# Optimization experiments

Measured on AMD Instinct MI355X. Metric: run time of the kernel, lower is better.

## Reference

```python
import jax, jax.numpy as jnp
import numpy as np

S, H, I, E, K = 16384, 1024, 512, 64, 2
CAP = 640  # capacity per expert: ceil(S*K/E * 1.25)


def setup_inputs() -> dict:
    key = jax.random.key(0)
    k0, k1, k2, k3, k4 = jax.random.split(key, 5)
    x = jax.random.normal(k0, (S, H), jnp.float32)
    w_gate = jax.random.normal(k1, (H, E), jnp.float32) * 0.02
    wg = jax.random.normal(k2, (E, H, I), jnp.float32) * 0.02
    wu = jax.random.normal(k3, (E, H, I), jnp.float32) * 0.02
    wd = jax.random.normal(k4, (E, I, H), jnp.float32) * 0.02
    return {"x": x, "w_gate": w_gate, "wg": wg, "wu": wu, "wd": wd}


def reference(x, w_gate, wg, wu, wd):
    # --- gate (fp32) + softmax ---
    logits = x.astype(jnp.float32) @ w_gate                      # [S,E]
    prob = jax.nn.softmax(logits, axis=-1)
    topk_p, topk_e = jax.lax.top_k(prob, K)                      # [S,K]

    # --- capacity-based dispatch (token-major, route-minor order, as in torch loop) ---
    flat_e = topk_e.reshape(-1)                                  # [S*K]
    onehot = jax.nn.one_hot(flat_e, E, dtype=jnp.int32)          # [S*K,E]
    pos = jnp.cumsum(onehot, axis=0)[jnp.arange(S * K), flat_e] - 1  # slot within expert
    valid = pos < CAP                                            # [S*K]

    combine_w = jnp.where(valid.reshape(S, K), topk_p, 0.0)      # dropped -> 0 weight
    slot_idx = jnp.where(valid, flat_e * CAP + pos, E * CAP)     # dummy row for drops
    x_rep = jnp.repeat(x, K, axis=0)                             # [S*K,H], row i = x[i//K]
    y = jnp.zeros((E * CAP + 1, H), x.dtype).at[slot_idx].set(x_rep)[: E * CAP]
    dispatched = y.reshape(E, CAP, H)

    # --- per-expert SwiGLU MLP (grouped GEMMs) ---
    g = jnp.einsum("ech,ehi->eci", dispatched, wg)
    u = jnp.einsum("ech,ehi->eci", dispatched, wu)
    expert_out = jnp.einsum("eci,eih->ech", jax.nn.silu(g) * u, wd)  # [E,CAP,H]

    # --- normalize weights and combine (gather + weighted sum) ---
    cw = combine_w / jnp.clip(combine_w.sum(-1, keepdims=True), 1e-12, None)
    scatter_index = jnp.where(valid, flat_e * CAP + pos, -1).reshape(S, K)
    gathered = expert_out.reshape(E * CAP, H)[scatter_index]     # [S,K,H]; -1 wraps, weight=0
    out = jnp.einsum("sk,skh->sh", cw, gathered)                 # [S,H]

    router_loss = jnp.zeros((1,), jnp.float32)
    return out, cw, router_loss, logits
```

## Files before the change

### kernel.cpp

```cpp
#include <hip/hip_runtime.h>
#include <hip/hip_bf16.h>

constexpr int S_TOK = 16384;
constexpr int HDIM  = 1024;
constexpr int IDIM  = 512;
constexpr int NEXP  = 64;
constexpr int CAPC  = 640;
constexpr int NCHUNK = 128;

typedef __attribute__((ext_vector_type(8))) short bf16x8;
typedef __attribute__((ext_vector_type(4))) short short4v;
typedef __attribute__((ext_vector_type(16))) float f32x16;

__device__ __forceinline__ float bf2f(unsigned short u){
  return __uint_as_float(((unsigned)u) << 16);
}
__device__ __forceinline__ unsigned short f2bf(float f){
  unsigned u = __float_as_uint(f);
  return (unsigned short)((u + 0x7fffu + ((u >> 16) & 1u)) >> 16);
}
__device__ __forceinline__ unsigned pk2cvt(float a, float b){
  unsigned r;
  asm volatile("v_cvt_pk_bf16_f32 %0, %1, %2" : "=v"(r) : "v"(a), "v"(b));
  return r;
}
__device__ __forceinline__ void gload_lds16(const void* g, void* l){
  __builtin_amdgcn_global_load_lds((const __attribute__((address_space(1))) unsigned*)g,
                                   (__attribute__((address_space(3))) unsigned*)l, 16, 0, 0);
}
__device__ __forceinline__ unsigned ldsoff(const void* p){ return (unsigned)(size_t)p; }
__device__ __forceinline__ void trread2(unsigned addr, short4v& lo, short4v& hi){
  asm volatile("ds_read_b64_tr_b16 %0, %2\n\t"
               "ds_read_b64_tr_b16 %1, %2 offset:128"
               : "=&v"(lo), "=&v"(hi) : "v"(addr));
}

__global__ __launch_bounds__(256) void gate_kernel(
    const float* __restrict__ x, const float* __restrict__ wgate,
    float* __restrict__ logits_out, float* __restrict__ topk_p,
    int* __restrict__ flat_e, float* __restrict__ rl_out)
{
  __shared__ float xs[4][HDIM];
  const int w = threadIdx.x >> 6, lane = threadIdx.x & 63;
  const int tok = blockIdx.x * 4 + w;
  const float4* xr = (const float4*)(x + (size_t)tok * HDIM);
  float4* xd = (float4*)(&xs[w][0]);
#pragma unroll
  for (int j = 0; j < 4; ++j) xd[j * 64 + lane] = xr[j * 64 + lane];
  __syncthreads();
  float acc = 0.f;
#pragma unroll 8
  for (int h = 0; h < HDIM; ++h)
    acc = fmaf(xs[w][h], wgate[h * NEXP + lane], acc);
  logits_out[(size_t)tok * NEXP + lane] = acc;
  float m = acc;
#pragma unroll
  for (int d = 1; d < 64; d <<= 1) m = fmaxf(m, __shfl_xor(m, d));
  float p = expf(acc - m);
  float sum = p;
#pragma unroll
  for (int d = 1; d < 64; d <<= 1) sum += __shfl_xor(sum, d);
  float prob = p / sum;
  float v = prob; int idx = lane;
#pragma unroll
  for (int d = 1; d < 64; d <<= 1){
    float ov = __shfl_xor(v, d); int oi = __shfl_xor(idx, d);
    if (ov > v || (ov == v && oi < idx)){ v = ov; idx = oi; }
  }
  const int e1 = idx; const float p1 = v;
  v = (lane == e1) ? -1.f : prob; idx = lane;
#pragma unroll
  for (int d = 1; d < 64; d <<= 1){
    float ov = __shfl_xor(v, d); int oi = __shfl_xor(idx, d);
    if (ov > v || (ov == v && oi < idx)){ v = ov; idx = oi; }
  }
  if (lane == 0){
    flat_e[tok * 2]     = e1;  flat_e[tok * 2 + 1] = idx;
    topk_p[tok * 2]     = p1;  topk_p[tok * 2 + 1] = v;
  }
  if (tok == 0 && lane == 0) rl_out[0] = 0.f;
}

__global__ __launch_bounds__(256) void hist_kernel(const int* __restrict__ flat_e,
                                                   int* __restrict__ counts)
{
  __shared__ int hh[NEXP];
  const int t = threadIdx.x;
  if (t < NEXP) hh[t] = 0;
  __syncthreads();
  const int e = flat_e[blockIdx.x * 256 + t];
  atomicAdd(&hh[e], 1);
  __syncthreads();
  if (t < NEXP) counts[blockIdx.x * NEXP + t] = hh[t];
}

__global__ __launch_bounds__(256) void offsets_kernel(const int* __restrict__ counts,
                                                      int* __restrict__ offs,
                                                      int* __restrict__ etot)
{
  const int w = threadIdx.x >> 6, lane = threadIdx.x & 63;
  const int e = blockIdx.x * 4 + w;
  int v0 = counts[lane * NEXP + e];
  int v1 = counts[(64 + lane) * NEXP + e];
  int s0 = v0, s1 = v1;
#pragma unroll
  for (int d = 1; d < 64; d <<= 1){
    int n0 = __shfl_up(s0, d); if (lane >= d) s0 += n0;
    int n1 = __shfl_up(s1, d); if (lane >= d) s1 += n1;
  }
  const int tot0 = __shfl(s0, 63);
  offs[lane * NEXP + e]        = s0 - v0;
  offs[(64 + lane) * NEXP + e] = tot0 + s1 - v1;
  if (lane == 63) etot[e] = tot0 + s1;
}

__global__ __launch_bounds__(256) void place_kernel(
    const int* __restrict__ flat_e, const float* __restrict__ topk_p,
    const int* __restrict__ offs, int* __restrict__ entry_slot,
    int* __restrict__ token_of_slot, float* __restrict__ cw_out)
{
  __shared__ int es[256];
  __shared__ float wsh[256];
  const int t = threadIdx.x;
  const int i = blockIdx.x * 256 + t;
  const int e = flat_e[i];
  es[t] = e;
  __syncthreads();
  int local = 0;
  for (int j = 0; j < t; ++j) local += (es[j] == e);
  const int pos = offs[blockIdx.x * NEXP + e] + local;
  const bool valid = pos < CAPC;
  const int slot = e * CAPC + pos;
  entry_slot[i] = valid ? slot : -1;
  if (valid) token_of_slot[slot] = i >> 1;
  const float p = topk_p[i];
  wsh[t] = valid ? p : 0.f;
  __syncthreads();
  const float wme = wsh[t], wo = wsh[t ^ 1];
  cw_out[i] = wme / fmaxf(wme + wo, 1e-12f);
}

__global__ __launch_bounds__(256) void adisp_kernel(
    const float* __restrict__ x, const int* __restrict__ token_of_slot,
    const int* __restrict__ etot, unsigned short* __restrict__ adisp)
{
  const int slot = blockIdx.x;
  const int e = slot / CAPC, c = slot - e * CAPC;
  int cnt = etot[e]; if (cnt > CAPC) cnt = CAPC;
  if (c >= cnt) return;
  const int tok = token_of_slot[slot];
  const int t = threadIdx.x;
  float4 v = ((const float4*)(x + (size_t)tok * HDIM))[t];
  ushort4 o; o.x = f2bf(v.x); o.y = f2bf(v.y); o.z = f2bf(v.z); o.w = f2bf(v.w);
  ((ushort4*)(adisp + (size_t)slot * HDIM))[t] = o;
}


__global__ __launch_bounds__(512, 2) void gemm1_kernel(
    const unsigned short* __restrict__ adisp,
    const float* __restrict__ wg, const float* __restrict__ wu,
    const int* __restrict__ etot,
    unsigned short* __restrict__ hbuf)
{
  constexpr int NK1 = HDIM / 32;
  __shared__ unsigned short As[3][128 * 32];
  __shared__ unsigned short Bs[3][2 * 128 * 32];
  const int bb = blockIdx.x;
  const int lb = (bb & 7) * 160 + (bb >> 3);
  const int e = lb / 20; const int r2 = lb - e * 20;
  const int nt = r2 / 5, mt = r2 - nt * 5;
  { int cnt = etot[e]; if (cnt > CAPC) cnt = CAPC;
    if (mt * 128 >= cnt) return; }
  const int t = threadIdx.x, w = t >> 6, lane = t & 63;
  const int wr = w >> 2, wc = w & 3;
  const size_t arow0 = (size_t)e * CAPC + (size_t)mt * 128;
  const unsigned short* abase = adisp + arow0 * HDIM;
  const float* gsrc = wg + (size_t)e * HDIM * IDIM + nt * 128;
  const float* usrc = wu + (size_t)e * HDIM * IDIM + nt * 128;

  int aoff; { int row = t >> 2, jsrc = (t & 3) ^ ((row >> 1) & 3);
              aoff = row * HDIM + jsrc * 8; }
  const int ks_ = w >> 2, khalf = (w >> 1) & 1, par = w & 1;
  const int dk = (lane >> 1) & 3, h8 = lane & 1;
  const int n16 = (lane >> 3) & 1, n32 = lane >> 4;
  const int bk = 16 * ks_ + 8 * khalf + 4 * par + dk;
  const int bn0 = n32 * 32 + n16 * 16 + h8 * 8;
  const int bgo = bk * IDIM + bn0;
  const unsigned bwo = (unsigned)(n32 * 1024 + ks_ * 512 + (khalf * 2 + n16) * 128
                                  + par * 64 + dk * 16 + h8 * 8);

  f32x16 ag[2], au[2];
#pragma unroll
  for (int i = 0; i < 2; ++i)
#pragma unroll
    for (int q = 0; q < 16; ++q){ ag[i][q] = 0.f; au[i][q] = 0.f; }

  float4 g0a, g0b, u0a, u0b, g1a, g1b, u1a, u1b;

#define G1_LOAD(KB, RA, RB, RC, RD) {                                          \
    const float* gp_ = gsrc + (size_t)(KB) * IDIM + bgo;                       \
    const float* up_ = usrc + (size_t)(KB) * IDIM + bgo;                       \
    RA = *(const float4*)gp_;       RB = *(const float4*)(gp_ + 4);            \
    RC = *(const float4*)up_;       RD = *(const float4*)(up_ + 4); }

#define G1_STORE(NB, WA, WB, WC, WD) {                                         \
    *(uint4*)&Bs[NB][bwo] = make_uint4(pk2cvt(WA.x,WA.y), pk2cvt(WA.z,WA.w),   \
                                       pk2cvt(WB.x,WB.y), pk2cvt(WB.z,WB.w));  \
    *(uint4*)&Bs[NB][4096 + bwo] = make_uint4(pk2cvt(WC.x,WC.y), pk2cvt(WC.z,WC.w), \
                                       pk2cvt(WD.x,WD.y), pk2cvt(WD.z,WD.w)); }

#define G1_STEP(TI, LA, LB, LC, LD, WA, WB, WC, WD) {                          \
    const int cur_ = (TI) % 3;                                                 \
    const bool pf_ = (TI) + 2 < NK1;                                           \
    if (pf_){                                                                  \
      const int kb2_ = ((TI) + 2) * 32;                                        \
      gload_lds16(abase + aoff + kb2_, &As[((TI) + 2) % 3][w * 64 * 8]);       \
      G1_LOAD(kb2_, LA, LB, LC, LD);                                           \
    }                                                                          \
    const unsigned b0_ = ldsoff(&Bs[cur_][0]) + (unsigned)wc * 2048            \
                         + (unsigned)(lane >> 4) * 256 + (unsigned)(lane & 15) * 8; \
    _Pragma("unroll")                                                          \
    for (int ksi = 0; ksi < 2; ++ksi){                                         \
      bf16x8 af0_, af1_, bg_, bu_;                                             \
      { int row0_ = wr * 64 + (lane & 31);                                     \
        int row1_ = row0_ + 32;                                                \
        int koct_ = ksi * 2 + (lane >> 5);                                     \
        af0_ = *(const bf16x8*)&As[cur_][row0_ * 32 + ((koct_ ^ ((row0_ >> 1) & 3)) * 8)]; \
        af1_ = *(const bf16x8*)&As[cur_][row1_ * 32 + ((koct_ ^ ((row1_ >> 1) & 3)) * 8)]; } \
      { short4v l0_, l1_, m0_, m1_;                                            \
        trread2(b0_ + (unsigned)ksi * 1024, l0_, l1_);                         \
        bg_ = __builtin_shufflevector(l0_, l1_, 0,1,2,3,4,5,6,7);              \
        trread2(b0_ + 8192 + (unsigned)ksi * 1024, m0_, m1_);                  \
        bu_ = __builtin_shufflevector(m0_, m1_, 0,1,2,3,4,5,6,7); }            \
      asm volatile("s_waitcnt lgkmcnt(0)" ::: "memory");                       \
      __builtin_amdgcn_sched_barrier(0);                                       \
      __builtin_amdgcn_s_setprio(1);                                           \
      ag[0] = __builtin_amdgcn_mfma_f32_32x32x16_bf16(af0_, bg_, ag[0], 0, 0, 0); \
      au[0] = __builtin_amdgcn_mfma_f32_32x32x16_bf16(af0_, bu_, au[0], 0, 0, 0); \
      ag[1] = __builtin_amdgcn_mfma_f32_32x32x16_bf16(af1_, bg_, ag[1], 0, 0, 0); \
      au[1] = __builtin_amdgcn_mfma_f32_32x32x16_bf16(af1_, bu_, au[1], 0, 0, 0); \
      __builtin_amdgcn_s_setprio(0);                                           \
    }                                                                          \
    if ((TI) + 1 < NK1){                                                       \
      if (pf_) asm volatile("s_waitcnt vmcnt(5)" ::: "memory");                \
      else     asm volatile("s_waitcnt vmcnt(0)" ::: "memory");                \
      G1_STORE(((TI) + 1) % 3, WA, WB, WC, WD);                                \
    }                                                                          \
    asm volatile("s_waitcnt lgkmcnt(0)" ::: "memory");                         \
    __builtin_amdgcn_s_barrier();                                              \
    __builtin_amdgcn_sched_barrier(0);                                         \
  }

  gload_lds16(abase + aoff + 0,  &As[0][w * 64 * 8]);
  G1_LOAD(0,  g0a, g0b, u0a, u0b);
  gload_lds16(abase + aoff + 32, &As[1][w * 64 * 8]);
  G1_LOAD(32, g1a, g1b, u1a, u1b);
  asm volatile("s_waitcnt vmcnt(5)" ::: "memory");
  G1_STORE(0, g0a, g0b, u0a, u0b);
  asm volatile("s_waitcnt lgkmcnt(0)" ::: "memory");
  __builtin_amdgcn_s_barrier();

  for (int tb = 0; tb < NK1; tb += 2){
    G1_STEP(tb,     g0a, g0b, u0a, u0b,  g1a, g1b, u1a, u1b);
    G1_STEP(tb + 1, g1a, g1b, u1a, u1b,  g0a, g0b, u0a, u0b);
  }
#undef G1_STEP
#undef G1_STORE
#undef G1_LOAD

#pragma unroll
  for (int mp = 0; mp < 2; ++mp)
#pragma unroll
    for (int r = 0; r < 16; ++r){
      int row = wr * 64 + mp * 32 + (r & 3) + 8 * (r >> 2) + 4 * (lane >> 5);
      int col = nt * 128 + wc * 32 + (lane & 31);
      float gv = ag[mp][r], uv = au[mp][r];
      float hv = gv / (1.f + expf(-gv)) * uv;
      hbuf[(arow0 + row) * IDIM + col] = f2bf(hv);
    }
}

__global__ __launch_bounds__(512, 2) void gemm2_kernel(
    const unsigned short* __restrict__ hbuf,
    const float* __restrict__ wd,
    const int* __restrict__ etot,
    unsigned short* __restrict__ eo)
{
  constexpr int NK2 = IDIM / 32;
  __shared__ unsigned short As[3][128 * 32];
  __shared__ unsigned short Bs[3][2 * 128 * 32];
  const int bb = blockIdx.x;
  const int lb = (bb & 7) * 160 + (bb >> 3);
  const int e = lb / 20; const int r2 = lb - e * 20;
  const int nt = r2 / 5, mt = r2 - nt * 5;
  { int cnt = etot[e]; if (cnt > CAPC) cnt = CAPC;
    if (mt * 128 >= cnt) return; }
  const int t = threadIdx.x, w = t >> 6, lane = t & 63;
  const int wr = w >> 2, wc = w & 3;
  const size_t arow0 = (size_t)e * CAPC + (size_t)mt * 128;
  const unsigned short* abase = hbuf + arow0 * IDIM;
  const float* dsrc = wd + (size_t)e * IDIM * HDIM + nt * 256;

  int aoff; { int row = t >> 2, jsrc = (t & 3) ^ ((row >> 1) & 3);
              aoff = row * IDIM + jsrc * 8; }
  const int ks_ = w >> 2, khalf = (w >> 1) & 1, par = w & 1;
  const int dk = (lane >> 1) & 3, h8 = lane & 1;
  const int n16 = (lane >> 3) & 1, n32 = lane >> 4;
  const int bk = 16 * ks_ + 8 * khalf + 4 * par + dk;
  const int bn0 = n32 * 32 + n16 * 16 + h8 * 8;
  const int bgo = bk * HDIM + bn0;
  const unsigned bwo = (unsigned)(n32 * 1024 + ks_ * 512 + (khalf * 2 + n16) * 128
                                  + par * 64 + dk * 16 + h8 * 8);

  f32x16 ac[2][2];
#pragma unroll
  for (int i = 0; i < 2; ++i)
#pragma unroll
    for (int j = 0; j < 2; ++j)
#pragma unroll
      for (int q = 0; q < 16; ++q) ac[i][j][q] = 0.f;

  float4 p0a, p0b, p1a, p1b, q0a, q0b, q1a, q1b;

#define G2_LOAD(KB, RA, RB, RC, RD) {                                          \
    const float* gp_ = dsrc + (size_t)(KB) * HDIM + bgo;                       \
    RA = *(const float4*)gp_;         RB = *(const float4*)(gp_ + 4);          \
    RC = *(const float4*)(gp_ + 128); RD = *(const float4*)(gp_ + 132); }

#define G2_STORE(NB, WA, WB, WC, WD) {                                         \
    *(uint4*)&Bs[NB][bwo] = make_uint4(pk2cvt(WA.x,WA.y), pk2cvt(WA.z,WA.w),   \
                                       pk2cvt(WB.x,WB.y), pk2cvt(WB.z,WB.w));  \
    *(uint4*)&Bs[NB][4096 + bwo] = make_uint4(pk2cvt(WC.x,WC.y), pk2cvt(WC.z,WC.w), \
                                       pk2cvt(WD.x,WD.y), pk2cvt(WD.z,WD.w)); }

#define G2_STEP(TI, LA, LB, LC, LD, WA, WB, WC, WD) {                          \
    const int cur_ = (TI) % 3;                                                 \
    const bool pf_ = (TI) + 2 < NK2;                                           \
    if (pf_){                                                                  \
      const int kb2_ = ((TI) + 2) * 32;                                        \
      gload_lds16(abase + aoff + kb2_, &As[((TI) + 2) % 3][w * 64 * 8]);       \
      G2_LOAD(kb2_, LA, LB, LC, LD);                                           \
    }                                                                          \
    const unsigned b0_ = ldsoff(&Bs[cur_][0]) + (unsigned)wc * 4096            \
                         + (unsigned)(lane >> 4) * 256 + (unsigned)(lane & 15) * 8; \
    _Pragma("unroll")                                                          \
    for (int ksi = 0; ksi < 2; ++ksi){                                         \
      bf16x8 af0_, af1_, b0f_, b1f_;                                           \
      { int row0_ = wr * 64 + (lane & 31);                                     \
        int row1_ = row0_ + 32;                                                \
        int koct_ = ksi * 2 + (lane >> 5);                                     \
        af0_ = *(const bf16x8*)&As[cur_][row0_ * 32 + ((koct_ ^ ((row0_ >> 1) & 3)) * 8)]; \
        af1_ = *(const bf16x8*)&As[cur_][row1_ * 32 + ((koct_ ^ ((row1_ >> 1) & 3)) * 8)]; } \
      { short4v l0_, l1_, m0_, m1_;                                            \
        trread2(b0_ + (unsigned)ksi * 1024, l0_, l1_);                         \
        b0f_ = __builtin_shufflevector(l0_, l1_, 0,1,2,3,4,5,6,7);             \
        trread2(b0_ + 2048 + (unsigned)ksi * 1024, m0_, m1_);                  \
        b1f_ = __builtin_shufflevector(m0_, m1_, 0,1,2,3,4,5,6,7); }           \
      asm volatile("s_waitcnt lgkmcnt(0)" ::: "memory");                       \
      __builtin_amdgcn_sched_barrier(0);                                       \
      __builtin_amdgcn_s_setprio(1);                                           \
      ac[0][0] = __builtin_amdgcn_mfma_f32_32x32x16_bf16(af0_, b0f_, ac[0][0], 0, 0, 0); \
      ac[0][1] = __builtin_amdgcn_mfma_f32_32x32x16_bf16(af0_, b1f_, ac[0][1], 0, 0, 0); \
      ac[1][0] = __builtin_amdgcn_mfma_f32_32x32x16_bf16(af1_, b0f_, ac[1][0], 0, 0, 0); \
      ac[1][1] = __builtin_amdgcn_mfma_f32_32x32x16_bf16(af1_, b1f_, ac[1][1], 0, 0, 0); \
      __builtin_amdgcn_s_setprio(0);                                           \
    }                                                                          \
    if ((TI) + 1 < NK2){                                                       \
      if (pf_) asm volatile("s_waitcnt vmcnt(5)" ::: "memory");                \
      else     asm volatile("s_waitcnt vmcnt(0)" ::: "memory");                \
      G2_STORE(((TI) + 1) % 3, WA, WB, WC, WD);                                \
    }                                                                          \
    asm volatile("s_waitcnt lgkmcnt(0)" ::: "memory");                         \
    __builtin_amdgcn_s_barrier();                                              \
    __builtin_amdgcn_sched_barrier(0);                                         \
  }

  gload_lds16(abase + aoff + 0,  &As[0][w * 64 * 8]);
  G2_LOAD(0,  p0a, p0b, q0a, q0b);
  gload_lds16(abase + aoff + 32, &As[1][w * 64 * 8]);
  G2_LOAD(32, p1a, p1b, q1a, q1b);
  asm volatile("s_waitcnt vmcnt(5)" ::: "memory");
  G2_STORE(0, p0a, p0b, q0a, q0b);
  asm volatile("s_waitcnt lgkmcnt(0)" ::: "memory");
  __builtin_amdgcn_s_barrier();

  for (int tb = 0; tb < NK2; tb += 2){
    G2_STEP(tb,     p0a, p0b, q0a, q0b,  p1a, p1b, q1a, q1b);
    G2_STEP(tb + 1, p1a, p1b, q1a, q1b,  p0a, p0b, q0a, q0b);
  }
#undef G2_STEP
#undef G2_STORE
#undef G2_LOAD

#pragma unroll
  for (int mp = 0; mp < 2; ++mp)
#pragma unroll
    for (int np = 0; np < 2; ++np)
#pragma unroll
      for (int r = 0; r < 16; ++r){
        int row = wr * 64 + mp * 32 + (r & 3) + 8 * (r >> 2) + 4 * (lane >> 5);
        int col = nt * 256 + wc * 64 + np * 32 + (lane & 31);
        eo[(arow0 + row) * HDIM + col] = f2bf(ac[mp][np][r]);
      }
}

__global__ __launch_bounds__(256) void combine_kernel(
    const unsigned short* __restrict__ eo, const int* __restrict__ entry_slot,
    const float* __restrict__ cw, float* __restrict__ out)
{
  const int s = blockIdx.x, t = threadIdx.x;
  const int s0 = entry_slot[2 * s], s1 = entry_slot[2 * s + 1];
  const float w0 = cw[2 * s], w1 = cw[2 * s + 1];
  const int c = t * 4;
  float r0 = 0.f, r1 = 0.f, r2 = 0.f, r3 = 0.f;
  if (s0 >= 0){
    ushort4 vq = *(const ushort4*)&eo[(size_t)s0 * HDIM + c];
    r0 += w0 * bf2f(vq.x); r1 += w0 * bf2f(vq.y); r2 += w0 * bf2f(vq.z); r3 += w0 * bf2f(vq.w);
  }
  if (s1 >= 0){
    ushort4 vq = *(const ushort4*)&eo[(size_t)s1 * HDIM + c];
    r0 += w1 * bf2f(vq.x); r1 += w1 * bf2f(vq.y); r2 += w1 * bf2f(vq.z); r3 += w1 * bf2f(vq.w);
  }
  ((float4*)(out + (size_t)s * HDIM))[t] = make_float4(r0, r1, r2, r3);
}

extern "C" void kernel_launch(void* const* d_in, const int* in_sizes, int n_in,
                              void* d_out, int out_size, void* d_ws, size_t ws_size,
                              hipStream_t stream) {
  (void)in_sizes; (void)n_in; (void)out_size; (void)ws_size;
  const float* x     = (const float*)d_in[0];
  const float* wgate = (const float*)d_in[1];
  const float* wg    = (const float*)d_in[2];
  const float* wu    = (const float*)d_in[3];
  const float* wd    = (const float*)d_in[4];

  float* out        = (float*)d_out;
  float* cw_out     = out + (size_t)S_TOK * HDIM;
  float* rl_out     = cw_out + (size_t)S_TOK * 2;
  float* logits_out = rl_out + 1;

  char* w8 = (char*)d_ws;
  size_t off = 0;
  auto alloc = [&](size_t bytes){ size_t r = off; off += (bytes + 255) & ~(size_t)255; return r; };
  int*   flat_e_ws        = (int*)  (w8 + alloc((size_t)32768 * 4));
  float* topk_p_ws        = (float*)(w8 + alloc((size_t)32768 * 4));
  int*   counts_ws        = (int*)  (w8 + alloc((size_t)NCHUNK * NEXP * 4));
  int*   offs_ws          = (int*)  (w8 + alloc((size_t)NCHUNK * NEXP * 4));
  int*   etot_ws          = (int*)  (w8 + alloc((size_t)NEXP * 4));
  int*   entry_slot_ws    = (int*)  (w8 + alloc((size_t)32768 * 4));
  int*   token_of_slot_ws = (int*)  (w8 + alloc((size_t)NEXP * CAPC * 4));
  unsigned short* hbuf_ws = (unsigned short*)(w8 + alloc((size_t)NEXP * CAPC * IDIM * 2));
  unsigned short* adisp_ws= (unsigned short*)(w8 + alloc((size_t)NEXP * CAPC * HDIM * 2));
  unsigned short* eo_ws   = adisp_ws;

  gate_kernel   <<<S_TOK / 4, 256, 0, stream>>>(x, wgate, logits_out, topk_p_ws, flat_e_ws, rl_out);
  hist_kernel   <<<NCHUNK,    256, 0, stream>>>(flat_e_ws, counts_ws);
  offsets_kernel<<<16,        256, 0, stream>>>(counts_ws, offs_ws, etot_ws);
  place_kernel  <<<NCHUNK,    256, 0, stream>>>(flat_e_ws, topk_p_ws, offs_ws,
                                                entry_slot_ws, token_of_slot_ws, cw_out);
  adisp_kernel  <<<NEXP * CAPC, 256, 0, stream>>>(x, token_of_slot_ws, etot_ws, adisp_ws);
  gemm1_kernel  <<<NEXP * 20, 512, 0, stream>>>(adisp_ws, wg, wu, etot_ws, hbuf_ws);
  gemm2_kernel  <<<NEXP * 20, 512, 0, stream>>>(hbuf_ws, wd, etot_ws, eo_ws);
  combine_kernel<<<S_TOK,     256, 0, stream>>>(eo_ws, entry_slot_ws, cw_out, out);
}
```

Before: 514.4 us.

## Enlarge grouped-GEMM M tile to 256 rows and split gate dot-product accumulators

Both expert GEMM kernels now use 256-row M tiles (3 M-tiles per expert instead of 5), with each wave computing four 32-row MFMA fragments. This halves how often the fp32 weight tiles are reloaded and converted per expert, which is where most global traffic comes from. The cost is more accumulator registers, dropping the 2-blocks-per-CU launch bound, more LDS, padded rows beyond capacity being clamped and skipped, and fewer blocks in the grid. The gate kernel also splits its dot product into four independent accumulators to shorten the FMA dependency chain.

```diff
diff --git a/kernel.cpp b/kernel.cpp
--- a/kernel.cpp
+++ b/kernel.cpp
@@ -48,10 +48,15 @@
 #pragma unroll
   for (int j = 0; j < 4; ++j) xd[j * 64 + lane] = xr[j * 64 + lane];
   __syncthreads();
-  float acc = 0.f;
-#pragma unroll 8
-  for (int h = 0; h < HDIM; ++h)
-    acc = fmaf(xs[w][h], wgate[h * NEXP + lane], acc);
+  float a0 = 0.f, a1 = 0.f, a2 = 0.f, a3 = 0.f;
+#pragma unroll 4
+  for (int h = 0; h < HDIM; h += 4){
+    a0 = fmaf(xs[w][h],     wgate[(h)     * NEXP + lane], a0);
+    a1 = fmaf(xs[w][h + 1], wgate[(h + 1) * NEXP + lane], a1);
+    a2 = fmaf(xs[w][h + 2], wgate[(h + 2) * NEXP + lane], a2);
+    a3 = fmaf(xs[w][h + 3], wgate[(h + 3) * NEXP + lane], a3);
+  }
+  float acc = (a0 + a1) + (a2 + a3);
   logits_out[(size_t)tok * NEXP + lane] = acc;
   float m = acc;
 #pragma unroll
@@ -156,30 +161,37 @@
 }
 
 
-__global__ __launch_bounds__(512, 2) void gemm1_kernel(
+__global__ __launch_bounds__(512) void gemm1_kernel(
     const unsigned short* __restrict__ adisp,
     const float* __restrict__ wg, const float* __restrict__ wu,
     const int* __restrict__ etot,
     unsigned short* __restrict__ hbuf)
 {
   constexpr int NK1 = HDIM / 32;
-  __shared__ unsigned short As[3][128 * 32];
+  __shared__ unsigned short As[3][256 * 32];
   __shared__ unsigned short Bs[3][2 * 128 * 32];
   const int bb = blockIdx.x;
-  const int lb = (bb & 7) * 160 + (bb >> 3);
-  const int e = lb / 20; const int r2 = lb - e * 20;
-  const int nt = r2 / 5, mt = r2 - nt * 5;
+  const int lb = (bb & 7) * 96 + (bb >> 3);
+  const int e = lb / 12; const int r2 = lb - e * 12;
+  const int nt = r2 / 3, mt = r2 - nt * 3;
   { int cnt = etot[e]; if (cnt > CAPC) cnt = CAPC;
-    if (mt * 128 >= cnt) return; }
+    if (mt * 256 >= cnt) return; }
   const int t = threadIdx.x, w = t >> 6, lane = t & 63;
   const int wr = w >> 2, wc = w & 3;
-  const size_t arow0 = (size_t)e * CAPC + (size_t)mt * 128;
+  const size_t arow0 = (size_t)e * CAPC + (size_t)mt * 256;
   const unsigned short* abase = adisp + arow0 * HDIM;
   const float* gsrc = wg + (size_t)e * HDIM * IDIM + nt * 128;
   const float* usrc = wu + (size_t)e * HDIM * IDIM + nt * 128;
 
-  int aoff; { int row = t >> 2, jsrc = (t & 3) ^ ((row >> 1) & 3);
-              aoff = row * HDIM + jsrc * 8; }
+  int aoff[2];
+#pragma unroll
+  for (int rr = 0; rr < 2; ++rr){
+    int c = rr * 512 + t;
+    int row = c >> 2;
+    if (mt * 256 + row >= CAPC) row = 0;
+    int jsrc = (c & 3) ^ ((row >> 1) & 3);
+    aoff[rr] = row * HDIM + jsrc * 8;
+  }
   const int ks_ = w >> 2, khalf = (w >> 1) & 1, par = w & 1;
   const int dk = (lane >> 1) & 3, h8 = lane & 1;
   const int n16 = (lane >> 3) & 1, n32 = lane >> 4;
@@ -189,9 +201,9 @@
   const unsigned bwo = (unsigned)(n32 * 1024 + ks_ * 512 + (khalf * 2 + n16) * 128
                                   + par * 64 + dk * 16 + h8 * 8);
 
-  f32x16 ag[2], au[2];
-#pragma unroll
-  for (int i = 0; i < 2; ++i)
+  f32x16 ag[4], au[4];
+#pragma unroll
+  for (int i = 0; i < 4; ++i)
 #pragma unroll
     for (int q = 0; q < 16; ++q){ ag[i][q] = 0.f; au[i][q] = 0.f; }
 
@@ -214,19 +226,21 @@
     const bool pf_ = (TI) + 2 < NK1;                                           \
     if (pf_){                                                                  \
       const int kb2_ = ((TI) + 2) * 32;                                        \
-      gload_lds16(abase + aoff + kb2_, &As[((TI) + 2) % 3][w * 64 * 8]);       \
+      gload_lds16(abase + aoff[0] + kb2_, &As[((TI) + 2) % 3][(w * 64) * 8]);  \
+      gload_lds16(abase + aoff[1] + kb2_, &As[((TI) + 2) % 3][(512 + w * 64) * 8]); \
       G1_LOAD(kb2_, LA, LB, LC, LD);                                           \
     }                                                                          \
     const unsigned b0_ = ldsoff(&Bs[cur_][0]) + (unsigned)wc * 2048            \
                          + (unsigned)(lane >> 4) * 256 + (unsigned)(lane & 15) * 8; \
     _Pragma("unroll")                                                          \
     for (int ksi = 0; ksi < 2; ++ksi){                                         \
-      bf16x8 af0_, af1_, bg_, bu_;                                             \
-      { int row0_ = wr * 64 + (lane & 31);                                     \
-        int row1_ = row0_ + 32;                                                \
-        int koct_ = ksi * 2 + (lane >> 5);                                     \
-        af0_ = *(const bf16x8*)&As[cur_][row0_ * 32 + ((koct_ ^ ((row0_ >> 1) & 3)) * 8)]; \
-        af1_ = *(const bf16x8*)&As[cur_][row1_ * 32 + ((koct_ ^ ((row1_ >> 1) & 3)) * 8)]; } \
+      bf16x8 af_[4], bg_, bu_;                                                 \
+      { int koct_ = ksi * 2 + (lane >> 5);                                     \
+        _Pragma("unroll")                                                      \
+        for (int mp = 0; mp < 4; ++mp){                                        \
+          int row_ = wr * 128 + mp * 32 + (lane & 31);                         \
+          af_[mp] = *(const bf16x8*)&As[cur_][row_ * 32 + ((koct_ ^ ((row_ >> 1) & 3)) * 8)]; \
+        } }                                                                    \
       { short4v l0_, l1_, m0_, m1_;                                            \
         trread2(b0_ + (unsigned)ksi * 1024, l0_, l1_);                         \
         bg_ = __builtin_shufflevector(l0_, l1_, 0,1,2,3,4,5,6,7);              \
@@ -235,14 +249,15 @@
       asm volatile("s_waitcnt lgkmcnt(0)" ::: "memory");                       \
       __builtin_amdgcn_sched_barrier(0);                                       \
       __builtin_amdgcn_s_setprio(1);                                           \
-      ag[0] = __builtin_amdgcn_mfma_f32_32x32x16_bf16(af0_, bg_, ag[0], 0, 0, 0); \
-      au[0] = __builtin_amdgcn_mfma_f32_32x32x16_bf16(af0_, bu_, au[0], 0, 0, 0); \
-      ag[1] = __builtin_amdgcn_mfma_f32_32x32x16_bf16(af1_, bg_, ag[1], 0, 0, 0); \
-      au[1] = __builtin_amdgcn_mfma_f32_32x32x16_bf16(af1_, bu_, au[1], 0, 0, 0); \
+      _Pragma("unroll")                                                        \
+      for (int mp = 0; mp < 4; ++mp){                                          \
+        ag[mp] = __builtin_amdgcn_mfma_f32_32x32x16_bf16(af_[mp], bg_, ag[mp], 0, 0, 0); \
+        au[mp] = __builtin_amdgcn_mfma_f32_32x32x16_bf16(af_[mp], bu_, au[mp], 0, 0, 0); \
+      }                                                                        \
       __builtin_amdgcn_s_setprio(0);                                           \
     }                                                                          \
     if ((TI) + 1 < NK1){                                                       \
-      if (pf_) asm volatile("s_waitcnt vmcnt(5)" ::: "memory");                \
+      if (pf_) asm volatile("s_waitcnt vmcnt(6)" ::: "memory");                \
       else     asm volatile("s_waitcnt vmcnt(0)" ::: "memory");                \
       G1_STORE(((TI) + 1) % 3, WA, WB, WC, WD);                                \
     }                                                                          \
@@ -251,11 +266,13 @@
     __builtin_amdgcn_sched_barrier(0);                                         \
   }
 
-  gload_lds16(abase + aoff + 0,  &As[0][w * 64 * 8]);
+  gload_lds16(abase + aoff[0] + 0,  &As[0][(w * 64) * 8]);
+  gload_lds16(abase + aoff[1] + 0,  &As[0][(512 + w * 64) * 8]);
   G1_LOAD(0,  g0a, g0b, u0a, u0b);
-  gload_lds16(abase + aoff + 32, &As[1][w * 64 * 8]);
+  gload_lds16(abase + aoff[0] + 32, &As[1][(w * 64) * 8]);
+  gload_lds16(abase + aoff[1] + 32, &As[1][(512 + w * 64) * 8]);
   G1_LOAD(32, g1a, g1b, u1a, u1b);
-  asm volatile("s_waitcnt vmcnt(5)" ::: "memory");
+  asm volatile("s_waitcnt vmcnt(6)" ::: "memory");
   G1_STORE(0, g0a, g0b, u0a, u0b);
   asm volatile("s_waitcnt lgkmcnt(0)" ::: "memory");
   __builtin_amdgcn_s_barrier();
@@ -269,10 +286,11 @@
 #undef G1_LOAD
 
 #pragma unroll
-  for (int mp = 0; mp < 2; ++mp)
+  for (int mp = 0; mp < 4; ++mp)
 #pragma unroll
     for (int r = 0; r < 16; ++r){
-      int row = wr * 64 + mp * 32 + (r & 3) + 8 * (r >> 2) + 4 * (lane >> 5);
+      int row = wr * 128 + mp * 32 + (r & 3) + 8 * (r >> 2) + 4 * (lane >> 5);
+      if (mt * 256 + row >= CAPC) continue;
       int col = nt * 128 + wc * 32 + (lane & 31);
       float gv = ag[mp][r], uv = au[mp][r];
       float hv = gv / (1.f + expf(-gv)) * uv;
@@ -280,29 +298,36 @@
     }
 }
 
-__global__ __launch_bounds__(512, 2) void gemm2_kernel(
+__global__ __launch_bounds__(512) void gemm2_kernel(
     const unsigned short* __restrict__ hbuf,
     const float* __restrict__ wd,
     const int* __restrict__ etot,
     unsigned short* __restrict__ eo)
 {
   constexpr int NK2 = IDIM / 32;
-  __shared__ unsigned short As[3][128 * 32];
+  __shared__ unsigned short As[3][256 * 32];
   __shared__ unsigned short Bs[3][2 * 128 * 32];
   const int bb = blockIdx.x;
-  const int lb = (bb & 7) * 160 + (bb >> 3);
-  const int e = lb / 20; const int r2 = lb - e * 20;
-  const int nt = r2 / 5, mt = r2 - nt * 5;
+  const int lb = (bb & 7) * 96 + (bb >> 3);
+  const int e = lb / 12; const int r2 = lb - e * 12;
+  const int nt = r2 / 3, mt = r2 - nt * 3;
   { int cnt = etot[e]; if (cnt > CAPC) cnt = CAPC;
-    if (mt * 128 >= cnt) return; }
+    if (mt * 256 >= cnt) return; }
   const int t = threadIdx.x, w = t >> 6, lane = t & 63;
   const int wr = w >> 2, wc = w & 3;
-  const size_t arow0 = (size_t)e * CAPC + (size_t)mt * 128;
+  const size_t arow0 = (size_t)e * CAPC + (size_t)mt * 256;
   const unsigned short* abase = hbuf + arow0 * IDIM;
   const float* dsrc = wd + (size_t)e * IDIM * HDIM + nt * 256;
 
-  int aoff; { int row = t >> 2, jsrc = (t & 3) ^ ((row >> 1) & 3);
-              aoff = row * IDIM + jsrc * 8; }
+  int aoff[2];
+#pragma unroll
+  for (int rr = 0; rr < 2; ++rr){
+    int c = rr * 512 + t;
+    int row = c >> 2;
+    if (mt * 256 + row >= CAPC) row = 0;
+    int jsrc = (c & 3) ^ ((row >> 1) & 3);
+    aoff[rr] = row * IDIM + jsrc * 8;
+  }
   const int ks_ = w >> 2, khalf = (w >> 1) & 1, par = w & 1;
   const int dk = (lane >> 1) & 3, h8 = lane & 1;
   const int n16 = (lane >> 3) & 1, n32 = lane >> 4;
@@ -312,9 +337,9 @@
   const unsigned bwo = (unsigned)(n32 * 1024 + ks_ * 512 + (khalf * 2 + n16) * 128
                                   + par * 64 + dk * 16 + h8 * 8);
 
-  f32x16 ac[2][2];
-#pragma unroll
-  for (int i = 0; i < 2; ++i)
+  f32x16 ac[4][2];
+#pragma unroll
+  for (int i = 0; i < 4; ++i)
 #pragma unroll
     for (int j = 0; j < 2; ++j)
 #pragma unroll
@@ -338,19 +363,21 @@
     const bool pf_ = (TI) + 2 < NK2;                                           \
     if (pf_){                                                                  \
       const int kb2_ = ((TI) + 2) * 32;                                        \
-      gload_lds16(abase + aoff + kb2_, &As[((TI) + 2) % 3][w * 64 * 8]);       \
+      gload_lds16(abase + aoff[0] + kb2_, &As[((TI) + 2) % 3][(w * 64) * 8]);  \
+      gload_lds16(abase + aoff[1] + kb2_, &As[((TI) + 2) % 3][(512 + w * 64) * 8]); \
       G2_LOAD(kb2_, LA, LB, LC, LD);                                           \
     }                                                                          \
     const unsigned b0_ = ldsoff(&Bs[cur_][0]) + (unsigned)wc * 4096            \
                          + (unsigned)(lane >> 4) * 256 + (unsigned)(lane & 15) * 8; \
     _Pragma("unroll")                                                          \
     for (int ksi = 0; ksi < 2; ++ksi){                                         \
-      bf16x8 af0_, af1_, b0f_, b1f_;                                           \
-      { int row0_ = wr * 64 + (lane & 31);                                     \
-        int row1_ = row0_ + 32;                                                \
-        int koct_ = ksi * 2 + (lane >> 5);                                     \
-        af0_ = *(const bf16x8*)&As[cur_][row0_ * 32 + ((koct_ ^ ((row0_ >> 1) & 3)) * 8)]; \
-        af1_ = *(const bf16x8*)&As[cur_][row1_ * 32 + ((koct_ ^ ((row1_ >> 1) & 3)) * 8)]; } \
+      bf16x8 af_[4], b0f_, b1f_;                                               \
+      { int koct_ = ksi * 2 + (lane >> 5);                                     \
+        _Pragma("unroll")                                                      \
+        for (int mp = 0; mp < 4; ++mp){                                        \
+          int row_ = wr * 128 + mp * 32 + (lane & 31);                         \
+          af_[mp] = *(const bf16x8*)&As[cur_][row_ * 32 + ((koct_ ^ ((row_ >> 1) & 3)) * 8)]; \
+        } }                                                                    \
       { short4v l0_, l1_, m0_, m1_;                                            \
         trread2(b0_ + (unsigned)ksi * 1024, l0_, l1_);                         \
         b0f_ = __builtin_shufflevector(l0_, l1_, 0,1,2,3,4,5,6,7);             \
@@ -359,14 +386,15 @@
       asm volatile("s_waitcnt lgkmcnt(0)" ::: "memory");                       \
       __builtin_amdgcn_sched_barrier(0);                                       \
       __builtin_amdgcn_s_setprio(1);                                           \
-      ac[0][0] = __builtin_amdgcn_mfma_f32_32x32x16_bf16(af0_, b0f_, ac[0][0], 0, 0, 0); \
-      ac[0][1] = __builtin_amdgcn_mfma_f32_32x32x16_bf16(af0_, b1f_, ac[0][1], 0, 0, 0); \
-      ac[1][0] = __builtin_amdgcn_mfma_f32_32x32x16_bf16(af1_, b0f_, ac[1][0], 0, 0, 0); \
-      ac[1][1] = __builtin_amdgcn_mfma_f32_32x32x16_bf16(af1_, b1f_, ac[1][1], 0, 0, 0); \
+      _Pragma("unroll")                                                        \
+      for (int mp = 0; mp < 4; ++mp){                                          \
+        ac[mp][0] = __builtin_amdgcn_mfma_f32_32x32x16_bf16(af_[mp], b0f_, ac[mp][0], 0, 0, 0); \
+        ac[mp][1] = __builtin_amdgcn_mfma_f32_32x32x16_bf16(af_[mp], b1f_, ac[mp][1], 0, 0, 0); \
+      }                                                                        \
       __builtin_amdgcn_s_setprio(0);                                           \
     }                                                                          \
     if ((TI) + 1 < NK2){                                                       \
-      if (pf_) asm volatile("s_waitcnt vmcnt(5)" ::: "memory");                \
+      if (pf_) asm volatile("s_waitcnt vmcnt(6)" ::: "memory");                \
       else     asm volatile("s_waitcnt vmcnt(0)" ::: "memory");                \
       G2_STORE(((TI) + 1) % 3, WA, WB, WC, WD);                                \
     }                                                                          \
@@ -375,11 +403,13 @@
     __builtin_amdgcn_sched_barrier(0);                                         \
   }
 
-  gload_lds16(abase + aoff + 0,  &As[0][w * 64 * 8]);
+  gload_lds16(abase + aoff[0] + 0,  &As[0][(w * 64) * 8]);
+  gload_lds16(abase + aoff[1] + 0,  &As[0][(512 + w * 64) * 8]);
   G2_LOAD(0,  p0a, p0b, q0a, q0b);
-  gload_lds16(abase + aoff + 32, &As[1][w * 64 * 8]);
+  gload_lds16(abase + aoff[0] + 32, &As[1][(w * 64) * 8]);
+  gload_lds16(abase + aoff[1] + 32, &As[1][(512 + w * 64) * 8]);
   G2_LOAD(32, p1a, p1b, q1a, q1b);
-  asm volatile("s_waitcnt vmcnt(5)" ::: "memory");
+  asm volatile("s_waitcnt vmcnt(6)" ::: "memory");
   G2_STORE(0, p0a, p0b, q0a, q0b);
   asm volatile("s_waitcnt lgkmcnt(0)" ::: "memory");
   __builtin_amdgcn_s_barrier();
@@ -393,12 +423,13 @@
 #undef G2_LOAD
 
 #pragma unroll
-  for (int mp = 0; mp < 2; ++mp)
+  for (int mp = 0; mp < 4; ++mp)
 #pragma unroll
     for (int np = 0; np < 2; ++np)
 #pragma unroll
       for (int r = 0; r < 16; ++r){
-        int row = wr * 64 + mp * 32 + (r & 3) + 8 * (r >> 2) + 4 * (lane >> 5);
+        int row = wr * 128 + mp * 32 + (r & 3) + 8 * (r >> 2) + 4 * (lane >> 5);
+        if (mt * 256 + row >= CAPC) continue;
         int col = nt * 256 + wc * 64 + np * 32 + (lane & 31);
         eo[(arow0 + row) * HDIM + col] = f2bf(ac[mp][np][r]);
       }
@@ -459,7 +490,7 @@
   place_kernel  <<<NCHUNK,    256, 0, stream>>>(flat_e_ws, topk_p_ws, offs_ws,
                                                 entry_slot_ws, token_of_slot_ws, cw_out);
   adisp_kernel  <<<NEXP * CAPC, 256, 0, stream>>>(x, token_of_slot_ws, etot_ws, adisp_ws);
-  gemm1_kernel  <<<NEXP * 20, 512, 0, stream>>>(adisp_ws, wg, wu, etot_ws, hbuf_ws);
-  gemm2_kernel  <<<NEXP * 20, 512, 0, stream>>>(hbuf_ws, wd, etot_ws, eo_ws);
+  gemm1_kernel  <<<NEXP * 12, 512, 0, stream>>>(adisp_ws, wg, wu, etot_ws, hbuf_ws);
+  gemm2_kernel  <<<NEXP * 12, 512, 0, stream>>>(hbuf_ws, wd, etot_ws, eo_ws);
   combine_kernel<<<S_TOK,     256, 0, stream>>>(eo_ws, entry_slot_ws, cw_out, out);
 }
```

New measurement: 483.9 us. 1.06x faster.
